# Optimization experiments

Hardware: AMD Instinct MI355X
Metric: run time of the kernel (lower is better)

## Reference

```python
import jax, jax.numpy as jnp
import numpy as np

L, C = 32768, 512
EPS = 1e-5

def _layernorm(x, w, b):
    mu = jnp.mean(x, axis=-1, keepdims=True)
    var = jnp.mean(jnp.square(x - mu), axis=-1, keepdims=True)
    return (x - mu) * jax.lax.rsqrt(var + EPS) * w + b

def _scan(u, decay):
    # inclusive first-order linear scan: b_t = decay * b_{t-1} + u_t
    a = jnp.broadcast_to(decay, u.shape)
    def combine(l, r):
        return (l[0] * r[0], r[1] + r[0] * l[1])
    _, b = jax.lax.associative_scan(combine, (a, u), axis=0)
    return b

def setup_inputs() -> dict:
    key = jax.random.key(0)
    ks = jax.random.split(key, 8)
    s = 0.02
    return {
        "x": jax.random.normal(ks[0], (L, C), dtype=jnp.float32),
        "ln1_w": jnp.ones((C,), jnp.float32),
        "ln1_b": jnp.zeros((C,), jnp.float32),
        "W_in": jax.random.normal(ks[1], (C, C), jnp.float32) * s,
        "b_in": jnp.zeros((C,), jnp.float32),
        "W_gate": jax.random.normal(ks[2], (C, C), jnp.float32) * s,
        "b_gate": jnp.zeros((C,), jnp.float32),
        "W_out": jax.random.normal(ks[3], (C, C), jnp.float32) * s,
        "b_out": jnp.zeros((C,), jnp.float32),
        "decay_logit": jnp.zeros((C,), jnp.float32),  # torch init: zeros -> sigmoid = 0.5
        "ln2_w": jnp.ones((C,), jnp.float32),
        "ln2_b": jnp.zeros((C,), jnp.float32),
        "W_ff1": jax.random.normal(ks[4], (C, 2 * C), jnp.float32) * s,
        "b_ff1": jnp.zeros((2 * C,), jnp.float32),
        "W_ff2": jax.random.normal(ks[5], (2 * C, C), jnp.float32) * s,
        "b_ff2": jnp.zeros((C,), jnp.float32),
    }

def reference(x, ln1_w, ln1_b, W_in, b_in, W_gate, b_gate, W_out, b_out,
              decay_logit, ln2_w, ln2_b, W_ff1, b_ff1, W_ff2, b_ff2):
    hidden = _layernorm(x, ln1_w, ln1_b)
    u = hidden @ W_in + b_in
    gate = jax.nn.sigmoid(hidden @ W_gate + b_gate)
    decay = jax.nn.sigmoid(decay_logit)
    fwd = _scan(u, decay) * gate
    bwd = jnp.flip(_scan(jnp.flip(u, axis=0), decay), axis=0) * gate
    state_out = 0.5 * (fwd + bwd)
    x = x + state_out @ W_out + b_out
    h = _layernorm(x, ln2_w, ln2_b)
    x = x + jax.nn.silu(h @ W_ff1 + b_ff1) @ W_ff2 + b_ff2
    return x
```

## Files before the change

### kernel.cpp

```cpp
#include <hip/hip_runtime.h>
#include <stdint.h>


#define L_SEQ 32768
#define CDIM 512
#define LN_EPS 1e-5f
#define CHUNK 64
#define NCHUNK (L_SEQ / CHUNK)
#define NGRP 16
#define GCHUNK (NCHUNK / NGRP)

typedef __attribute__((ext_vector_type(8))) short short8;
typedef __attribute__((ext_vector_type(4))) float floatx4;

__device__ inline unsigned short f2bf(float f) {
  union { float f; unsigned int u; } v; v.f = f;
  unsigned int r = v.u + 0x7fffu + ((v.u >> 16) & 1u);
  return (unsigned short)(r >> 16);
}
__device__ inline float bf2f(unsigned short h) {
  union { float f; unsigned int u; } v; v.u = ((unsigned int)h) << 16;
  return v.f;
}
__device__ inline float sigmoidf_(float x) { return 1.0f / (1.0f + __expf(-x)); }

__device__ inline float powi5(float s, int e) {
  float p = 1.f;
#pragma unroll
  for (int b = 0; b < 5; b++) { if (e & (1 << b)) p *= s; s *= s; }
  return p;
}

__device__ __forceinline__ void gll16(const void* g, void* l) {
  __builtin_amdgcn_global_load_lds(
      (__attribute__((address_space(1))) void*)g,
      (__attribute__((address_space(3))) void*)l, 16, 0, 0);
}

__global__ __launch_bounds__(256) void prep_ln1(
    const float* __restrict__ x, const float* __restrict__ ln1_w,
    const float* __restrict__ ln1_b, unsigned short* __restrict__ out,
    const float* __restrict__ W_in, const float* __restrict__ W_gate,
    const float* __restrict__ W_out, const float* __restrict__ W_ff1,
    const float* __restrict__ W_ff2, const float* __restrict__ logit,
    unsigned short* __restrict__ Wt_ig, unsigned short* __restrict__ Wt_out,
    unsigned short* __restrict__ Wt_ff1, unsigned short* __restrict__ Wt_ff2,
    float* __restrict__ decay, float* __restrict__ decayT) {
  int bx = blockIdx.x;
  if (bx < L_SEQ / 4) {
    int row = bx * 4 + (threadIdx.x >> 6);
    int lane = threadIdx.x & 63;
    const float4* xr = (const float4*)(x + (size_t)row * CDIM);
    float4 v0 = xr[lane * 2];
    float4 v1 = xr[lane * 2 + 1];
    float s = v0.x + v0.y + v0.z + v0.w + v1.x + v1.y + v1.z + v1.w;
    float s2 = v0.x * v0.x + v0.y * v0.y + v0.z * v0.z + v0.w * v0.w +
               v1.x * v1.x + v1.y * v1.y + v1.z * v1.z + v1.w * v1.w;
    for (int m = 32; m > 0; m >>= 1) {
      s += __shfl_xor(s, m, 64);
      s2 += __shfl_xor(s2, m, 64);
    }
    float mean = s * (1.0f / CDIM);
    float var = s2 * (1.0f / CDIM) - mean * mean;
    float rs = rsqrtf(var + LN_EPS);
    const float4* wr = (const float4*)ln1_w;
    const float4* br = (const float4*)ln1_b;
    float4 w0 = wr[lane * 2], w1 = wr[lane * 2 + 1];
    float4 b0 = br[lane * 2], b1 = br[lane * 2 + 1];
    unsigned int p0 = (unsigned int)f2bf((v0.x - mean) * rs * w0.x + b0.x) |
                      ((unsigned int)f2bf((v0.y - mean) * rs * w0.y + b0.y) << 16);
    unsigned int p1 = (unsigned int)f2bf((v0.z - mean) * rs * w0.z + b0.z) |
                      ((unsigned int)f2bf((v0.w - mean) * rs * w0.w + b0.w) << 16);
    unsigned int p2 = (unsigned int)f2bf((v1.x - mean) * rs * w1.x + b1.x) |
                      ((unsigned int)f2bf((v1.y - mean) * rs * w1.y + b1.y) << 16);
    unsigned int p3 = (unsigned int)f2bf((v1.z - mean) * rs * w1.z + b1.z) |
                      ((unsigned int)f2bf((v1.w - mean) * rs * w1.w + b1.w) << 16);
    uint4 pk; pk.x = p0; pk.y = p1; pk.z = p2; pk.w = p3;
    *((uint4*)(out + (size_t)row * CDIM + lane * 8)) = pk;
    return;
  }
  int b = bx - L_SEQ / 4;
  if (b >= 1792) {
    for (int c = threadIdx.x; c < CDIM; c += 256) {
      float d = sigmoidf_(logit[c]);
      decay[c] = d;
      float p = d;
      for (int i = 0; i < 6; i++) p *= p;
      decayT[c] = p;
    }
    return;
  }
  const float* W; unsigned short* Wt; int Kd, Nd, t;
  if (b < 256)       { W = W_in;   Wt = Wt_ig;             Kd = 512;  Nd = 512;  t = b; }
  else if (b < 512)  { W = W_gate; Wt = Wt_ig + 512 * 512; Kd = 512;  Nd = 512;  t = b - 256; }
  else if (b < 768)  { W = W_out;  Wt = Wt_out;            Kd = 512;  Nd = 512;  t = b - 512; }
  else if (b < 1280) { W = W_ff1;  Wt = Wt_ff1;            Kd = 512;  Nd = 1024; t = b - 768; }
  else               { W = W_ff2;  Wt = Wt_ff2;            Kd = 1024; Nd = 512;  t = b - 1280; }
  int ntx = Nd >> 5;
  int n0 = (t % ntx) * 32, k0 = (t / ntx) * 32;
  __shared__ float tile[32][33];
  int tx = threadIdx.x & 31, ty = threadIdx.x >> 5;
  for (int r = 0; r < 32; r += 8)
    tile[ty + r][tx] = W[(size_t)(k0 + ty + r) * Nd + n0 + tx];
  __syncthreads();
  for (int r = 0; r < 32; r += 8)
    Wt[(size_t)(n0 + ty + r) * Kd + k0 + tx] = f2bf(tile[tx][ty + r]);
}

__global__ __launch_bounds__(256) void ln_bf16(const unsigned short* __restrict__ xb,
    const float* __restrict__ w, const float* __restrict__ b,
    unsigned short* __restrict__ out) {
  int row = blockIdx.x * 4 + (threadIdx.x >> 6);
  int lane = threadIdx.x & 63;
  uint4 uv = *(const uint4*)(xb + (size_t)row * CDIM + lane * 8);
  float v[8];
  v[0] = bf2f((unsigned short)(uv.x & 0xffffu));
  v[1] = bf2f((unsigned short)(uv.x >> 16));
  v[2] = bf2f((unsigned short)(uv.y & 0xffffu));
  v[3] = bf2f((unsigned short)(uv.y >> 16));
  v[4] = bf2f((unsigned short)(uv.z & 0xffffu));
  v[5] = bf2f((unsigned short)(uv.z >> 16));
  v[6] = bf2f((unsigned short)(uv.w & 0xffffu));
  v[7] = bf2f((unsigned short)(uv.w >> 16));
  float s = 0.f, s2 = 0.f;
#pragma unroll
  for (int i = 0; i < 8; i++) { s += v[i]; s2 += v[i] * v[i]; }
  for (int m = 32; m > 0; m >>= 1) {
    s += __shfl_xor(s, m, 64);
    s2 += __shfl_xor(s2, m, 64);
  }
  float mean = s * (1.0f / CDIM);
  float var = s2 * (1.0f / CDIM) - mean * mean;
  float rs = rsqrtf(var + LN_EPS);
  const float4* wr = (const float4*)w;
  const float4* br = (const float4*)b;
  float4 w0 = wr[lane * 2], w1 = wr[lane * 2 + 1];
  float4 b0 = br[lane * 2], b1 = br[lane * 2 + 1];
  unsigned int p0 = (unsigned int)f2bf((v[0] - mean) * rs * w0.x + b0.x) |
                    ((unsigned int)f2bf((v[1] - mean) * rs * w0.y + b0.y) << 16);
  unsigned int p1 = (unsigned int)f2bf((v[2] - mean) * rs * w0.z + b0.z) |
                    ((unsigned int)f2bf((v[3] - mean) * rs * w0.w + b0.w) << 16);
  unsigned int p2 = (unsigned int)f2bf((v[4] - mean) * rs * w1.x + b1.x) |
                    ((unsigned int)f2bf((v[5] - mean) * rs * w1.y + b1.y) << 16);
  unsigned int p3 = (unsigned int)f2bf((v[6] - mean) * rs * w1.z + b1.z) |
                    ((unsigned int)f2bf((v[7] - mean) * rs * w1.w + b1.w) << 16);
  uint4 pk; pk.x = p0; pk.y = p1; pk.z = p2; pk.w = p3;
  *((uint4*)(out + (size_t)row * CDIM + lane * 8)) = pk;
}

template <int EPI>
__global__ __launch_bounds__(256, 4) void gemm_bt(
    const unsigned short* __restrict__ A, const unsigned short* __restrict__ Bt,
    const float* __restrict__ biasA, const float* __restrict__ biasB,
    const float* __restrict__ res, const unsigned short* __restrict__ resB,
    float* __restrict__ outF,
    unsigned short* __restrict__ outU, unsigned short* __restrict__ outG,
    const float* __restrict__ decayP, float* __restrict__ faP,
    float* __restrict__ baP, int M, int N, int K) {
  __shared__ char smemRaw[34048];
  unsigned short* As = (unsigned short*)smemRaw;
  unsigned short* Bs = (unsigned short*)(smemRaw + 16384);

  int nbx = gridDim.x, nby = gridDim.y;
  int bid = blockIdx.x + blockIdx.y * nbx;
  int per = (nbx * nby) >> 3;
  int w = (bid & 7) * per + (bid >> 3);
  int ni = w % nby;
  int mi = w / nby;
  int bm = mi << 7, bn = ni << 7;

  int tid = threadIdx.x, wave = tid >> 6, lane = tid & 63;
  int wm = (wave >> 1) * 64, wn = (wave & 1) * 64;

  int srow = wave * 16 + (lane >> 2);
  int chunkSel = (lane & 3) ^ ((lane >> 3) & 3);
  int scol = chunkSel * 8;
  const unsigned short* aP0 = A + (size_t)(bm + srow) * K + scol;
  const unsigned short* aP1 = A + (size_t)(bm + 64 + srow) * K + scol;
  const unsigned short* bP0 = Bt + (size_t)(bn + srow) * K + scol;
  const unsigned short* bP1 = Bt + (size_t)(bn + 64 + srow) * K + scol;
  int wbase = wave * 512;

#define STAGE(bufOff, ktile) do {                                 \
    int _o = (ktile) * 32;                                        \
    gll16(aP0 + _o, As + (bufOff) + wbase);                       \
    gll16(aP1 + _o, As + (bufOff) + 2048 + wbase);                \
    gll16(bP0 + _o, Bs + (bufOff) + wbase);                       \
    gll16(bP1 + _o, Bs + (bufOff) + 2048 + wbase);                \
  } while (0)

  floatx4 acc[4][4];
#pragma unroll
  for (int i = 0; i < 4; i++)
#pragma unroll
    for (int j = 0; j < 4; j++) acc[i][j] = (floatx4){0.f, 0.f, 0.f, 0.f};

  int quad = lane >> 4, r16 = lane & 15;
  int cSwz = ((quad ^ (r16 >> 1)) & 3) * 8;

  int NK = K >> 5;

  STAGE(0, 0);
  asm volatile("s_waitcnt vmcnt(0)" ::: "memory");
  __syncthreads();

  for (int k = 0; k < NK; ++k) {
    int cur = (k & 1) * 4096, nxt = cur ^ 4096;
    if (k + 1 < NK) STAGE(nxt, k + 1);
    short8 af[4], bfm[4];
#pragma unroll
    for (int i = 0; i < 4; i++)
      af[i] = *(const short8*)(&As[cur + (wm + i * 16 + r16) * 32 + cSwz]);
#pragma unroll
    for (int j = 0; j < 4; j++)
      bfm[j] = *(const short8*)(&Bs[cur + (wn + j * 16 + r16) * 32 + cSwz]);
#pragma unroll
    for (int i = 0; i < 4; i++)
#pragma unroll
      for (int j = 0; j < 4; j++)
        acc[i][j] = __builtin_amdgcn_mfma_f32_16x16x32_bf16(af[i], bfm[j], acc[i][j], 0, 0, 0);
    asm volatile("s_waitcnt vmcnt(0)" ::: "memory");
    __syncthreads();
  }
#undef STAGE

  if (EPI == 4) {
#pragma unroll
    for (int j = 0; j < 4; j++) {
      int n = bn + wn + j * 16 + r16;
      float bA = biasA[n];
#pragma unroll
      for (int i = 0; i < 4; i++) {
        int mb = bm + wm + i * 16 + quad * 4;
#pragma unroll
        for (int r = 0; r < 4; r++) {
          size_t idx = (size_t)(mb + r) * N + n;
          outF[idx] = bf2f(resB[idx]) + acc[i][j][r] + bA;
        }
      }
    }
  } else {
    unsigned short* sm = (unsigned short*)smemRaw;
#pragma unroll
    for (int j = 0; j < 4; j++) {
      int n = bn + wn + j * 16 + r16;
      int ln = wn + j * 16 + r16;
#pragma unroll
      for (int i = 0; i < 4; i++) {
        int lmb = wm + i * 16 + quad * 4;
#pragma unroll
        for (int r = 0; r < 4; r++) {
          float v = acc[i][j][r];
          float t;
          if (EPI == 0) {
            t = (n < 512) ? (v + biasA[n]) : sigmoidf_(v + biasB[n - 512]);
          } else if (EPI == 2) {
            float z = v + biasA[n];
            t = z * sigmoidf_(z);
          } else {
            size_t gidx = (size_t)(bm + lmb + r) * N + n;
            t = res[gidx] + v + biasA[n];
          }
          sm[(lmb + r) * 132 + ln] = f2bf(t);
        }
      }
    }
    __syncthreads();
    int row = tid >> 1, half = tid & 1;
    const unsigned short* src = sm + row * 132 + half * 64;
    unsigned short* gptr;
    if (EPI == 0) {
      gptr = ((bn < 512) ? outU : (outG - 512)) + (size_t)(bm + row) * 512 + bn + half * 64;
    } else {
      gptr = outG + (size_t)(bm + row) * N + bn + half * 64;
    }
#pragma unroll
    for (int s = 0; s < 8; s++)
      *(short8*)(gptr + s * 8) = *(const short8*)(src + s * 8);

    if (EPI == 0 && bn < 512 && faP != nullptr) {
      int cl = tid & 127;
      int ch = tid >> 7;
      int cg = bn + cl;
      float d = decayP[cg];
      const unsigned short* col = sm + (ch * 64) * 132 + cl;
      float f = 0.f, bs = 0.f, p = 1.f;
#pragma unroll 8
      for (int t = 0; t < CHUNK; t++) {
        float v = bf2f(col[t * 132]);
        f = d * f + v;
        bs += p * v;
        p *= d;
      }
      size_t kidx = (size_t)((bm >> 6) + ch) * CDIM + cg;
      faP[kidx] = f;
      baP[kidx] = bs;
    }
  }
}

__global__ __launch_bounds__(512) void scan_p2a(const float* __restrict__ fa,
    const float* __restrict__ ba, const float* __restrict__ decayT,
    float* __restrict__ fc, float* __restrict__ bc,
    float* __restrict__ gaF, float* __restrict__ gaB) {
  int c = threadIdx.x, g = blockIdx.x;
  float dT = decayT[c];
  int k0 = g * GCHUNK;
  float runf = 0.f;
#pragma unroll 4
  for (int j = 0; j < GCHUNK; j++) {
    size_t idx = (size_t)(k0 + j) * CDIM + c;
    fc[idx] = runf;
    runf = dT * runf + fa[idx];
  }
  gaF[(size_t)g * CDIM + c] = runf;
  float runb = 0.f;
#pragma unroll 4
  for (int j = GCHUNK - 1; j >= 0; j--) {
    size_t idx = (size_t)(k0 + j) * CDIM + c;
    bc[idx] = runb;
    runb = dT * runb + ba[idx];
  }
  gaB[(size_t)g * CDIM + c] = runb;
}

__global__ __launch_bounds__(512) void scan_p2b(const float* __restrict__ gaF,
    const float* __restrict__ gaB, const float* __restrict__ decayT,
    float* __restrict__ GF, float* __restrict__ GB) {
  int c = threadIdx.x;
  float dT = decayT[c];
  float d32 = dT;
#pragma unroll
  for (int i = 0; i < 5; i++) d32 *= d32;
  float gf = 0.f;
#pragma unroll
  for (int g = 0; g < NGRP; g++) {
    GF[(size_t)g * CDIM + c] = gf;
    gf = d32 * gf + gaF[(size_t)g * CDIM + c];
  }
  float gb = 0.f;
#pragma unroll
  for (int g = NGRP - 1; g >= 0; g--) {
    GB[(size_t)g * CDIM + c] = gb;
    gb = d32 * gb + gaB[(size_t)g * CDIM + c];
  }
}

__global__ __launch_bounds__(512) void scan_phase3(const unsigned short* __restrict__ u,
    const unsigned short* __restrict__ gate, const float* __restrict__ decay,
    const float* __restrict__ decayT, const float* __restrict__ fc,
    const float* __restrict__ bc, const float* __restrict__ GF,
    const float* __restrict__ GB, unsigned short* __restrict__ state) {
  int c = threadIdx.x, k = blockIdx.x;
  int g = k >> 5, j = k & 31;
  float d = decay[c];
  float dT = decayT[c];
  size_t base = (size_t)k * CHUNK * CDIM + c;
  size_t kc = (size_t)k * CDIM + c;
  size_t gc = (size_t)g * CDIM + c;
  float run  = fc[kc] + powi5(dT, j) * GF[gc];
  float runb0 = bc[kc] + powi5(dT, 31 - j) * GB[gc];
  float fwd[CHUNK];
  unsigned int us[CHUNK / 2];
#pragma unroll
  for (int t = 0; t < CHUNK; t++) {
    unsigned short uv = u[base + (size_t)t * CDIM];
    if (t & 1) us[t >> 1] |= ((unsigned int)uv) << 16;
    else       us[t >> 1] = uv;
    run = d * run + bf2f(uv);
    fwd[t] = run;
  }
  float runb = runb0;
#pragma unroll
  for (int t = CHUNK - 1; t >= 0; t--) {
    unsigned short uv = (unsigned short)((us[t >> 1] >> ((t & 1) * 16)) & 0xffffu);
    runb = d * runb + bf2f(uv);
    float gv = bf2f(gate[base + (size_t)t * CDIM]);
    state[base + (size_t)t * CDIM] = f2bf(0.5f * (fwd[t] + runb) * gv);
  }
}

extern "C" void kernel_launch(void* const* d_in, const int* in_sizes, int n_in,
                              void* d_out, int out_size, void* d_ws, size_t ws_size,
                              hipStream_t stream) {
  const float* x = (const float*)d_in[0];
  const float* ln1_w = (const float*)d_in[1];
  const float* ln1_b = (const float*)d_in[2];
  const float* W_in = (const float*)d_in[3];
  const float* b_in = (const float*)d_in[4];
  const float* W_gate = (const float*)d_in[5];
  const float* b_gate = (const float*)d_in[6];
  const float* W_out = (const float*)d_in[7];
  const float* b_out = (const float*)d_in[8];
  const float* decay_logit = (const float*)d_in[9];
  const float* ln2_w = (const float*)d_in[10];
  const float* ln2_b = (const float*)d_in[11];
  const float* W_ff1 = (const float*)d_in[12];
  const float* b_ff1 = (const float*)d_in[13];
  const float* W_ff2 = (const float*)d_in[14];
  const float* b_ff2 = (const float*)d_in[15];

  char* ws = (char*)d_ws;
  size_t off = 0;
  auto alloc = [&](size_t bytes) -> void* {
    void* p = ws + off;
    off += (bytes + 255) & ~(size_t)255;
    return p;
  };
  unsigned short* Wt_ig  = (unsigned short*)alloc((size_t)1024 * 512 * 2);
  unsigned short* Wt_out = (unsigned short*)alloc((size_t)512 * 512 * 2);
  unsigned short* Wt_ff1 = (unsigned short*)alloc((size_t)1024 * 512 * 2);
  unsigned short* Wt_ff2 = (unsigned short*)alloc((size_t)512 * 1024 * 2);
  float* fa = (float*)alloc((size_t)NCHUNK * CDIM * 4);
  float* ba = (float*)alloc((size_t)NCHUNK * CDIM * 4);
  float* fc = (float*)alloc((size_t)NCHUNK * CDIM * 4);
  float* bc = (float*)alloc((size_t)NCHUNK * CDIM * 4);
  float* gaF = (float*)alloc((size_t)NGRP * CDIM * 4);
  float* gaB = (float*)alloc((size_t)NGRP * CDIM * 4);
  float* GFb = (float*)alloc((size_t)NGRP * CDIM * 4);
  float* GBb = (float*)alloc((size_t)NGRP * CDIM * 4);
  float* decay  = (float*)alloc(CDIM * 4);
  float* decayT = (float*)alloc(CDIM * 4);
  const size_t LC2 = (size_t)L_SEQ * CDIM * 2;
  unsigned short* R1 = (unsigned short*)alloc(LC2);
  unsigned short* R2 = (unsigned short*)alloc(LC2);
  unsigned short* R3 = (unsigned short*)alloc(LC2);
  unsigned short* x2b = (unsigned short*)alloc(LC2);
  unsigned short* hidden = R1;
  unsigned short* state  = R1;
  unsigned short* hbuf   = R1;
  unsigned short* u_buf  = R2;
  unsigned short* gate   = R3;
  unsigned short* ffb    = R2;

  prep_ln1<<<L_SEQ / 4 + 1793, 256, 0, stream>>>(x, ln1_w, ln1_b, hidden,
      W_in, W_gate, W_out, W_ff1, W_ff2, decay_logit,
      Wt_ig, Wt_out, Wt_ff1, Wt_ff2, decay, decayT);

  gemm_bt<0><<<dim3(L_SEQ / 128, 1024 / 128), 256, 0, stream>>>(
      hidden, Wt_ig, b_in, b_gate, nullptr, nullptr, nullptr, u_buf, gate,
      decay, fa, ba, L_SEQ, 1024, 512);

  scan_p2a<<<NGRP, 512, 0, stream>>>(fa, ba, decayT, fc, bc, gaF, gaB);
  scan_p2b<<<1, 512, 0, stream>>>(gaF, gaB, decayT, GFb, GBb);
  scan_phase3<<<NCHUNK, 512, 0, stream>>>(u_buf, gate, decay, decayT, fc, bc,
      GFb, GBb, state);

  gemm_bt<3><<<dim3(L_SEQ / 128, 512 / 128), 256, 0, stream>>>(
      state, Wt_out, b_out, nullptr, x, nullptr, nullptr, nullptr, x2b,
      nullptr, nullptr, nullptr, L_SEQ, 512, 512);

  ln_bf16<<<L_SEQ / 4, 256, 0, stream>>>(x2b, ln2_w, ln2_b, hbuf);

  gemm_bt<2><<<dim3(L_SEQ / 128, 1024 / 128), 256, 0, stream>>>(
      hbuf, Wt_ff1, b_ff1, nullptr, nullptr, nullptr, nullptr, nullptr, ffb,
      nullptr, nullptr, nullptr, L_SEQ, 1024, 512);

  gemm_bt<4><<<dim3(L_SEQ / 128, 512 / 128), 256, 0, stream>>>(
      ffb, Wt_ff2, b_ff2, nullptr, nullptr, x2b, (float*)d_out, nullptr, nullptr,
      nullptr, nullptr, nullptr, L_SEQ, 512, 1024);
}
```

Baseline: 411.0 us.

## Compute chunk scan summaries from MFMA accumulators with 32-row chunks

The per-chunk forward and backward scan summaries are now computed directly from the fp32 GEMM accumulator registers using decay-power weights and cross-lane shuffles, instead of a serial 64-step loop over bf16 values staged in shared memory after the store. The chunk size is halved to 32 and the group count doubled to match the MFMA tile layout. This removes a serial per-thread loop from the GEMM epilogue and uses unrounded values, at the cost of more chunk summaries for the phase-2 and phase-3 scan kernels to process. The phase-3 code relies on a local array sized by CHUNK and on powi5 with a group size of 32, so consistency depends on code that is not shown.

```diff
diff --git a/kernel.cpp b/kernel.cpp
--- a/kernel.cpp
+++ b/kernel.cpp
@@ -5,9 +5,9 @@
 #define L_SEQ 32768
 #define CDIM 512
 #define LN_EPS 1e-5f
-#define CHUNK 64
+#define CHUNK 32
 #define NCHUNK (L_SEQ / CHUNK)
-#define NGRP 16
+#define NGRP 32
 #define GCHUNK (NCHUNK / NGRP)
 
 typedef __attribute__((ext_vector_type(8))) short short8;
@@ -85,7 +85,7 @@
       float d = sigmoidf_(logit[c]);
       decay[c] = d;
       float p = d;
-      for (int i = 0; i < 6; i++) p *= p;
+      for (int i = 0; i < 5; i++) p *= p;
       decayT[c] = p;
     }
     return;
@@ -240,6 +240,45 @@
       }
     }
   } else {
+    if (EPI == 0 && bn < 512 && faP != nullptr) {
+#pragma unroll
+      for (int j = 0; j < 4; j++) {
+        int n = bn + wn + j * 16 + r16;
+        float d = decayP[n];
+        float bb = biasA[n];
+        float dd2 = d * d, dd3 = dd2 * d;
+        float d4v = dd2 * dd2;
+        float d8v = d4v * d4v;
+        float d16v = d8v * d8v;
+        float dr[4] = {1.f, d, dd2, dd3};
+        float dq4v = 1.f, dqf4v = 1.f;
+        if (quad & 1) dq4v *= d4v; else dqf4v *= d4v;
+        if (quad & 2) dq4v *= d8v; else dqf4v *= d8v;
+        float f0 = 0.f, b0 = 0.f, f1 = 0.f, b1 = 0.f;
+#pragma unroll
+        for (int r = 0; r < 4; r++) {
+          float wb = dq4v * dr[r];
+          float wf = dqf4v * dr[3 - r];
+          float u00 = acc[0][j][r] + bb;
+          float u01 = acc[1][j][r] + bb;
+          float u10 = acc[2][j][r] + bb;
+          float u11 = acc[3][j][r] + bb;
+          b0 += wb * (u00 + d16v * u01);
+          f0 += wf * (d16v * u00 + u01);
+          b1 += wb * (u10 + d16v * u11);
+          f1 += wf * (d16v * u10 + u11);
+        }
+        f0 += __shfl_xor(f0, 16, 64); f0 += __shfl_xor(f0, 32, 64);
+        b0 += __shfl_xor(b0, 16, 64); b0 += __shfl_xor(b0, 32, 64);
+        f1 += __shfl_xor(f1, 16, 64); f1 += __shfl_xor(f1, 32, 64);
+        b1 += __shfl_xor(b1, 16, 64); b1 += __shfl_xor(b1, 32, 64);
+        if (quad == 0) {
+          size_t i0 = (size_t)((bm + wm) >> 5) * CDIM + n;
+          faP[i0] = f0; baP[i0] = b0;
+          faP[i0 + CDIM] = f1; baP[i0 + CDIM] = b1;
+        }
+      }
+    }
     unsigned short* sm = (unsigned short*)smemRaw;
 #pragma unroll
     for (int j = 0; j < 4; j++) {
@@ -277,25 +316,6 @@
 #pragma unroll
     for (int s = 0; s < 8; s++)
       *(short8*)(gptr + s * 8) = *(const short8*)(src + s * 8);
-
-    if (EPI == 0 && bn < 512 && faP != nullptr) {
-      int cl = tid & 127;
-      int ch = tid >> 7;
-      int cg = bn + cl;
-      float d = decayP[cg];
-      const unsigned short* col = sm + (ch * 64) * 132 + cl;
-      float f = 0.f, bs = 0.f, p = 1.f;
-#pragma unroll 8
-      for (int t = 0; t < CHUNK; t++) {
-        float v = bf2f(col[t * 132]);
-        f = d * f + v;
-        bs += p * v;
-        p *= d;
-      }
-      size_t kidx = (size_t)((bm >> 6) + ch) * CDIM + cg;
-      faP[kidx] = f;
-      baP[kidx] = bs;
-    }
   }
 }
 
@@ -329,20 +349,20 @@
     float* __restrict__ GF, float* __restrict__ GB) {
   int c = threadIdx.x;
   float dT = decayT[c];
-  float d32 = dT;
-#pragma unroll
-  for (int i = 0; i < 5; i++) d32 *= d32;
+  float dG = dT;
+#pragma unroll
+  for (int i = 0; i < 5; i++) dG *= dG;
   float gf = 0.f;
 #pragma unroll
   for (int g = 0; g < NGRP; g++) {
     GF[(size_t)g * CDIM + c] = gf;
-    gf = d32 * gf + gaF[(size_t)g * CDIM + c];
+    gf = dG * gf + gaF[(size_t)g * CDIM + c];
   }
   float gb = 0.f;
 #pragma unroll
   for (int g = NGRP - 1; g >= 0; g--) {
     GB[(size_t)g * CDIM + c] = gb;
-    gb = d32 * gb + gaB[(size_t)g * CDIM + c];
+    gb = dG * gb + gaB[(size_t)g * CDIM + c];
   }
 }
 
```

Measured after the change: 420.4 us. 1.02x slower.
